# Kernel tuning notes

Hardware: AMD Instinct MI355X
Metric: run time of the kernel (lower is better)

Reference implementation:

```python
import jax, jax.numpy as jnp
import numpy as np

N, DIM, H, W = 8, 64, 256, 256
K = 3            # strip kernel size
EPS = 1e-5       # BatchNorm eps


def setup_inputs() -> dict:
    key = jax.random.key(0)
    kx, kh, kw = jax.random.split(key, 3)
    x = jax.random.normal(kx, (N, DIM, H, W), jnp.float32)

    def branch_params(k):
        k1, k2, k3, k4, k5 = jax.random.split(k, 5)
        w = jax.random.normal(k1, (DIM * K, DIM), jnp.float32) / np.sqrt(DIM).astype(np.float32)
        g = jax.random.uniform(k2, (DIM * K,), jnp.float32, 0.5, 1.5)   # BN weight
        b = jax.random.normal(k3, (DIM * K,), jnp.float32) * 0.1       # BN bias
        m = jax.random.normal(k4, (DIM * K,), jnp.float32) * 0.1       # BN running_mean
        v = jax.random.uniform(k5, (DIM * K,), jnp.float32, 0.5, 1.5)  # BN running_var
        return w, g, b, m, v

    wH, gH, bH, mH, vH = branch_params(kh)
    wW, gW, bW, mW, vW = branch_params(kw)
    return dict(x=x, wH=wH, gH=gH, bH=bH, mH=mH, vH=vH,
                wW=wW, gW=gW, bW=bW, mW=mW, vW=vW)


def _strip_att(x, w, g, b, m, v, horizontal):
    # Dynamic per-sample, per-channel 1D strip filter (involution-style).
    n, c, h, wd = x.shape
    gap = x.mean(axis=(2, 3))                       # (n, c)  AdaptiveAvgPool2d(1,1)
    f = gap @ w.T                                   # (n, c*K) 1x1 conv, no bias
    f = (f - m) * (g / jnp.sqrt(v + EPS)) + b       # BatchNorm2d (eval mode)
    f = jnp.tanh(f).reshape(n, c, K)                # per-(sample,channel) kernel taps
    pad = (K - 1) // 2
    if horizontal:  # kernel (1, K), reflect-pad width
        xp = jnp.pad(x, ((0, 0), (0, 0), (0, 0), (pad, pad)), mode='reflect')
        win = jnp.stack([xp[..., j:j + wd] for j in range(K)], axis=-1)  # (n,c,h,w,K)
    else:           # kernel (K, 1), reflect-pad height
        xp = jnp.pad(x, ((0, 0), (0, 0), (pad, pad), (0, 0)), mode='reflect')
        win = jnp.stack([xp[:, :, j:j + h, :] for j in range(K)], axis=-1)
    # grouped conv with groups = n*dim == depthwise correlation with dynamic taps
    return jnp.einsum('nchwk,nck->nchw', win, f)


def reference(x, wH, gH, bH, mH, vH, wW, gW, bW, mW, vW):
    out1 = _strip_att(x, wH, gH, bH, mH, vH, True)   # H_spatial_att (1,K) kernel
    out2 = _strip_att(x, wW, gW, bW, mW, vW, False)  # W_spatial_att (K,1) kernel
    return jnp.concatenate((out1, out2), axis=1)     # (n, 2c, h, w)
```

## Files before the change

kernel.cpp:

```cpp
#include <hip/hip_runtime.h>
#include <math.h>

#define N 8
#define DIM 64
#define H 256
#define W 256
#define K 3
#define EPS 1e-5f
#define TH 32

__global__ __launch_bounds__(512) void gap_kernel(const float* __restrict__ x,
                                                  float* __restrict__ gap) {
    const int plane = blockIdx.x;
    const float4* p4 = (const float4*)(x + (size_t)plane * (H * W));
    const int tid = threadIdx.x;
    float s = 0.f;
    #pragma unroll 4
    for (int i = tid; i < (H * W) / 4; i += 512) {
        float4 v = p4[i];
        s += (v.x + v.y) + (v.z + v.w);
    }
    __shared__ float red[512];
    red[tid] = s;
    __syncthreads();
    for (int off = 256; off > 0; off >>= 1) {
        if (tid < off) red[tid] += red[tid + off];
        __syncthreads();
    }
    if (tid == 0) gap[plane] = red[0] * (1.0f / (H * W));
}

__global__ __launch_bounds__(256) void conv_kernel(const float* __restrict__ x,
                                                   const float* __restrict__ gap,
                                                   const float* __restrict__ wH,
                                                   const float* __restrict__ gH,
                                                   const float* __restrict__ bH,
                                                   const float* __restrict__ mH,
                                                   const float* __restrict__ vH,
                                                   const float* __restrict__ wW,
                                                   const float* __restrict__ gW,
                                                   const float* __restrict__ bW,
                                                   const float* __restrict__ mW,
                                                   const float* __restrict__ vW,
                                                   float* __restrict__ out) {
    __shared__ float tile[(TH + 2) * W];
    __shared__ float s_taps[6];

    const int plane = blockIdx.y;
    const int n = plane / DIM;
    const int c = plane % DIM;
    const int h0 = blockIdx.x * TH;
    const int tid = threadIdx.x;

    if (tid < 6) {
        const int br = tid / K;
        const int k  = tid % K;
        const int j  = c * K + k;
        const float* w = br ? wW : wH;
        const float* g = br ? gW : gH;
        const float* b = br ? bW : bH;
        const float* m = br ? mW : mH;
        const float* v = br ? vW : vH;
        const float* grow = gap + n * DIM;
        const float* wrow = w + (size_t)j * DIM;
        float acc = 0.f;
        #pragma unroll
        for (int d = 0; d < DIM; d++) acc += grow[d] * wrow[d];
        float f = (acc - m[j]) * (g[j] * rsqrtf(v[j] + EPS)) + b[j];
        s_taps[tid] = tanhf(f);
    }

    const float4* xp4 = (const float4*)(x + (size_t)plane * (H * W));
    float4* t4 = (float4*)tile;
    for (int idx = tid; idx < (TH + 2) * W / 4; idx += 256) {
        const int row = idx >> 6;
        int hh = h0 - 1 + row;
        if (hh < 0) hh = 1;
        else if (hh >= H) hh = 2 * H - 2 - hh;
        t4[idx] = xp4[hh * (W / 4) + (idx & 63)];
    }
    __syncthreads();

    const float tH0 = s_taps[0], tH1 = s_taps[1], tH2 = s_taps[2];
    const float tW0 = s_taps[3], tW1 = s_taps[4], tW2 = s_taps[5];

    const int tx = tid & 63;
    const int ty = tid >> 6;

    float4* o1 = (float4*)out + ((size_t)(n * 2 * DIM + c) * H + h0) * (W / 4);
    float4* o2 = (float4*)out + ((size_t)(n * 2 * DIM + DIM + c) * H + h0) * (W / 4);

    #pragma unroll
    for (int r = 0; r < TH / 4; r++) {
        const int row = r * 4 + ty;
        const float* rc = tile + (row + 1) * W;
        const float4 cc = ((const float4*)rc)[tx];
        const float4 up = ((const float4*)(tile + row * W))[tx];
        const float4 dn = ((const float4*)(tile + (row + 2) * W))[tx];
        const float lf = (tx == 0)  ? cc.y : rc[4 * tx - 1];
        const float rt = (tx == 63) ? cc.z : rc[4 * tx + 4];

        float4 r1, r2;
        r1.x = lf   * tH0 + cc.x * tH1 + cc.y * tH2;
        r1.y = cc.x * tH0 + cc.y * tH1 + cc.z * tH2;
        r1.z = cc.y * tH0 + cc.z * tH1 + cc.w * tH2;
        r1.w = cc.z * tH0 + cc.w * tH1 + rt   * tH2;

        r2.x = up.x * tW0 + cc.x * tW1 + dn.x * tW2;
        r2.y = up.y * tW0 + cc.y * tW1 + dn.y * tW2;
        r2.z = up.z * tW0 + cc.z * tW1 + dn.z * tW2;
        r2.w = up.w * tW0 + cc.w * tW1 + dn.w * tW2;

        o1[row * (W / 4) + tx] = r1;
        o2[row * (W / 4) + tx] = r2;
    }
}

extern "C" void kernel_launch(void* const* d_in, const int* in_sizes, int n_in,
                              void* d_out, int out_size, void* d_ws, size_t ws_size,
                              hipStream_t stream) {
    const float* x  = (const float*)d_in[0];
    const float* wH = (const float*)d_in[1];
    const float* gH = (const float*)d_in[2];
    const float* bH = (const float*)d_in[3];
    const float* mH = (const float*)d_in[4];
    const float* vH = (const float*)d_in[5];
    const float* wW = (const float*)d_in[6];
    const float* gW = (const float*)d_in[7];
    const float* bW = (const float*)d_in[8];
    const float* mW = (const float*)d_in[9];
    const float* vW = (const float*)d_in[10];
    float* out = (float*)d_out;

    float* gap = (float*)d_ws;

    gap_kernel<<<N * DIM, 512, 0, stream>>>(x, gap);

    dim3 grid(H / TH, N * DIM);
    conv_kernel<<<grid, 256, 0, stream>>>(x, gap, wH, gH, bH, mH, vH,
                                          wW, gW, bW, mW, vW, out);
}
```

Measured before the change: 402.9 us.

## Replace LDS tile with register rows, wave shuffles and nontemporal stores

The conv kernel no longer stages a (TH+2)-row tile in shared memory. Each thread loads its six needed rows straight into registers, gets horizontal neighbours through wavefront shuffles, and writes output with nontemporal stores. Rows per block drop from 32 to 16, which doubles the grid. This removes LDS traffic and the big shared allocation so occupancy can rise, at the cost of more redundant halo loads from global memory (6 rows read per 4 produced).

```diff
diff --git a/kernel.cpp b/kernel.cpp
--- a/kernel.cpp
+++ b/kernel.cpp
@@ -7,17 +7,19 @@
 #define W 256
 #define K 3
 #define EPS 1e-5f
-#define TH 32
+#define RT 16
+
+typedef float f4 __attribute__((ext_vector_type(4)));
 
 __global__ __launch_bounds__(512) void gap_kernel(const float* __restrict__ x,
                                                   float* __restrict__ gap) {
     const int plane = blockIdx.x;
-    const float4* p4 = (const float4*)(x + (size_t)plane * (H * W));
+    const f4* p4 = (const f4*)(x + (size_t)plane * (H * W));
     const int tid = threadIdx.x;
     float s = 0.f;
     #pragma unroll 4
     for (int i = tid; i < (H * W) / 4; i += 512) {
-        float4 v = p4[i];
+        f4 v = p4[i];
         s += (v.x + v.y) + (v.z + v.w);
     }
     __shared__ float red[512];
@@ -43,14 +45,15 @@
                                                    const float* __restrict__ mW,
                                                    const float* __restrict__ vW,
                                                    float* __restrict__ out) {
-    __shared__ float tile[(TH + 2) * W];
     __shared__ float s_taps[6];
 
     const int plane = blockIdx.y;
     const int n = plane / DIM;
     const int c = plane % DIM;
-    const int h0 = blockIdx.x * TH;
     const int tid = threadIdx.x;
+    const int tx = tid & 63;
+    const int ty = tid >> 6;
+    const int r0 = blockIdx.x * RT + ty * 4;
 
     if (tid < 6) {
         const int br = tid / K;
@@ -70,37 +73,34 @@
         s_taps[tid] = tanhf(f);
     }
 
-    const float4* xp4 = (const float4*)(x + (size_t)plane * (H * W));
-    float4* t4 = (float4*)tile;
-    for (int idx = tid; idx < (TH + 2) * W / 4; idx += 256) {
-        const int row = idx >> 6;
-        int hh = h0 - 1 + row;
+    const f4* xp4 = (const f4*)(x + (size_t)plane * (H * W));
+    f4 v[6];
+    #pragma unroll
+    for (int j = 0; j < 6; j++) {
+        int hh = r0 - 1 + j;
         if (hh < 0) hh = 1;
         else if (hh >= H) hh = 2 * H - 2 - hh;
-        t4[idx] = xp4[hh * (W / 4) + (idx & 63)];
+        v[j] = xp4[hh * (W / 4) + tx];
     }
     __syncthreads();
 
     const float tH0 = s_taps[0], tH1 = s_taps[1], tH2 = s_taps[2];
     const float tW0 = s_taps[3], tW1 = s_taps[4], tW2 = s_taps[5];
 
-    const int tx = tid & 63;
-    const int ty = tid >> 6;
-
-    float4* o1 = (float4*)out + ((size_t)(n * 2 * DIM + c) * H + h0) * (W / 4);
-    float4* o2 = (float4*)out + ((size_t)(n * 2 * DIM + DIM + c) * H + h0) * (W / 4);
+    f4* o1 = (f4*)out + ((size_t)(n * 2 * DIM + c) * H + r0) * (W / 4) + tx;
+    f4* o2 = (f4*)out + ((size_t)(n * 2 * DIM + DIM + c) * H + r0) * (W / 4) + tx;
 
     #pragma unroll
-    for (int r = 0; r < TH / 4; r++) {
-        const int row = r * 4 + ty;
-        const float* rc = tile + (row + 1) * W;
-        const float4 cc = ((const float4*)rc)[tx];
-        const float4 up = ((const float4*)(tile + row * W))[tx];
-        const float4 dn = ((const float4*)(tile + (row + 2) * W))[tx];
-        const float lf = (tx == 0)  ? cc.y : rc[4 * tx - 1];
-        const float rt = (tx == 63) ? cc.z : rc[4 * tx + 4];
+    for (int i = 0; i < 4; i++) {
+        const f4 up = v[i];
+        const f4 cc = v[i + 1];
+        const f4 dn = v[i + 2];
+        float lf = __shfl_up(cc.w, 1, 64);
+        float rt = __shfl_down(cc.x, 1, 64);
+        if (tx == 0)  lf = cc.y;
+        if (tx == 63) rt = cc.z;
 
-        float4 r1, r2;
+        f4 r1, r2;
         r1.x = lf   * tH0 + cc.x * tH1 + cc.y * tH2;
         r1.y = cc.x * tH0 + cc.y * tH1 + cc.z * tH2;
         r1.z = cc.y * tH0 + cc.z * tH1 + cc.w * tH2;
@@ -111,8 +111,8 @@
         r2.z = up.z * tW0 + cc.z * tW1 + dn.z * tW2;
         r2.w = up.w * tW0 + cc.w * tW1 + dn.w * tW2;
 
-        o1[row * (W / 4) + tx] = r1;
-        o2[row * (W / 4) + tx] = r2;
+        __builtin_nontemporal_store(r1, o1 + i * (W / 4));
+        __builtin_nontemporal_store(r2, o2 + i * (W / 4));
     }
 }
 
@@ -136,7 +136,7 @@
 
     gap_kernel<<<N * DIM, 512, 0, stream>>>(x, gap);
 
-    dim3 grid(H / TH, N * DIM);
+    dim3 grid(H / RT, N * DIM);
     conv_kernel<<<grid, 256, 0, stream>>>(x, gap, wH, gH, bH, mH, vH,
                                           wW, gW, bW, mW, vW, out);
 }
```

Measured after the change: 388.7 us. 3.5% less time.
